# Kernel tuning notes

Hardware: AMD Instinct MI355X
Metric: run time of the kernel (lower is better)

The kernel has to match this reference:

```python
import jax, jax.numpy as jnp
import numpy as np

B, S, H, NH, K = 8, 1024, 1024, 16, 512
HD = H // NH  # head dim = 64


def setup_inputs() -> dict:
    key = jax.random.key(0)
    ks = jax.random.split(key, 9)
    hidden_states = jax.random.normal(ks[0], (B, S, H), jnp.float32)
    # remain_layers: exactly K nonzero entries per row (static max_tokens = K)
    scores = jax.random.uniform(ks[1], (B, S))
    thresh = jnp.sort(scores, axis=1)[:, S - K][:, None]
    remain_layers = (scores >= thresh).astype(jnp.int32)
    attention_mask = jnp.zeros((B, 1, 1, S), jnp.float32)  # additive mask
    init = 0.02
    Wq = jax.random.normal(ks[2], (H, H), jnp.float32) * init
    bq = jnp.zeros((H,), jnp.float32)
    Wk = jax.random.normal(ks[3], (H, H), jnp.float32) * init
    bk = jnp.zeros((H,), jnp.float32)
    Wv = jax.random.normal(ks[4], (H, H), jnp.float32) * init
    bv = jnp.zeros((H,), jnp.float32)
    return {"hidden_states": hidden_states, "attention_mask": attention_mask,
            "remain_layers": remain_layers, "Wq": Wq, "bq": bq,
            "Wk": Wk, "bk": bk, "Wv": Wv, "bv": bv}


def _heads(x):  # [B, L, H] -> [B, NH, L, HD]
    b, l, _ = x.shape
    return x.reshape(b, l, NH, HD).transpose(0, 2, 1, 3)


def reference(hidden_states, attention_mask, remain_layers, Wq, bq, Wk, bk, Wv, bv):
    # get_reduced_hidden: per-row gather of tokens with remain_layers > 0,
    # in original position order, zero-padded to max_tokens (= K here).
    order = jnp.argsort(1 - remain_layers, axis=1, stable=True)  # nonzeros first, order kept
    idx = order[:, :K]                                           # [B, K]
    reduced = jnp.take_along_axis(hidden_states, idx[:, :, None], axis=1)  # [B, K, H]
    valid = (jnp.take_along_axis(remain_layers, idx, axis=1) > 0)
    reduced = reduced * valid[:, :, None].astype(reduced.dtype)  # zero-pad slots

    q = _heads(reduced @ Wq.T + bq)          # [B, NH, K, HD]
    k = _heads(hidden_states @ Wk.T + bk)    # [B, NH, S, HD]
    v = _heads(hidden_states @ Wv.T + bv)    # [B, NH, S, HD]

    scores = jnp.einsum('bhqd,bhkd->bhqk', q, k) / np.sqrt(HD).astype(np.float32)
    scores = scores + attention_mask         # additive mask broadcast
    probs = jax.nn.softmax(scores, axis=-1)  # dropout is identity at eval
    ctx = jnp.einsum('bhqk,bhkd->bhqd', probs, v)  # [B, NH, K, HD]
    ctx = ctx.transpose(0, 2, 1, 3).reshape(B, K, H)
    return ctx
```

## Files before the change

### kernel.cpp

```cpp
#include <hip/hip_runtime.h>
#include <hip/hip_bf16.h>
#include <stdint.h>

#define S_LEN 1024
#define HDIM  1024
#define NHEADS 16
#define HEAD_D 64
#define KSEL  512
#define BATCH 8

typedef unsigned short ushort_t;
typedef __attribute__((ext_vector_type(8))) __bf16 bf16x8;
typedef __attribute__((ext_vector_type(4))) float  f32x4;

typedef const __attribute__((address_space(1))) void cg_void;
typedef __attribute__((address_space(3))) void lds_void;

__device__ __forceinline__ void gl_lds16(const void* g, void* l) {
    __builtin_amdgcn_global_load_lds((cg_void*)g, (lds_void*)l, 16, 0, 0);
}

__device__ __forceinline__ ushort_t f2bf(float f) {
    union { float f; unsigned int i; } x; x.f = f;
    unsigned int r = (x.i + 0x7fffu + ((x.i >> 16) & 1u)) >> 16;
    return (ushort_t)r;
}

__global__ __launch_bounds__(1024) void prep_kernel(
    const float* __restrict__ hidden, const float* __restrict__ wq,
    const float* __restrict__ wk, const float* __restrict__ wv,
    const int* __restrict__ remain,
    ushort_t* __restrict__ hbf, ushort_t* __restrict__ wqb,
    ushort_t* __restrict__ wkb, ushort_t* __restrict__ wvb,
    short* __restrict__ pos, int* __restrict__ valid) {
    __shared__ int wsum[16];
    __shared__ int woff[17];
    int blk = blockIdx.x;
    if (blk < 2816) {
        const float* s; ushort_t* d; int base;
        if (blk < 2048)      { s = hidden; d = hbf; base = blk; }
        else if (blk < 2304) { s = wq; d = wqb; base = blk - 2048; }
        else if (blk < 2560) { s = wk; d = wkb; base = blk - 2304; }
        else                 { s = wv; d = wvb; base = blk - 2560; }
        int i = base * 1024 + threadIdx.x;
        float4 v = ((const float4*)s)[i];
        ushort4 o;
        o.x = f2bf(v.x); o.y = f2bf(v.y); o.z = f2bf(v.z); o.w = f2bf(v.w);
        ((ushort4*)d)[i] = o;
    } else {
        int b = blk - 2816, t = threadIdx.x;
        int r = remain[b * S_LEN + t];
        unsigned long long m = __ballot(r != 0);
        int lane = t & 63, w = t >> 6;
        int pre = __popcll(m & ((1ull << lane) - 1ull));
        if (lane == 0) wsum[w] = __popcll(m);
        __syncthreads();
        if (t == 0) { int a = 0; for (int i = 0; i < 16; i++) { woff[i] = a; a += wsum[i]; } woff[16] = a; }
        __syncthreads();
        int tot = woff[16];
        int onesBefore = woff[w] + pre;
        int slot = r ? onesBefore : (tot + (t - onesBefore));
        pos[b * S_LEN + t] = (short)((slot < KSEL) ? slot : -1);
        if (slot < KSEL) valid[b * KSEL + slot] = r;
    }
}

#define QSCALE 0.1803368801111244f
#define LT_PITCH 264
#define BAR() __asm__ volatile("s_barrier" ::: "memory")
#define VMCNT(n) __asm__ volatile("s_waitcnt vmcnt(" #n ")" ::: "memory")

#define GPHASE(mt0, ...) { \
    bf16x8 Af0, Af1, Af2, Af3; \
    { const ushort_t* ap = &pool[Ab + (mt0) * 1024 + aRow]; \
      Af0 = *(const bf16x8*)(ap + ksw0); \
      Af1 = *(const bf16x8*)(ap + ksw1); \
      Af2 = *(const bf16x8*)(ap + 1024 + ksw0); \
      Af3 = *(const bf16x8*)(ap + 1024 + ksw1); } \
    __VA_ARGS__; \
    BAR(); \
    __builtin_amdgcn_s_setprio(1); \
    _Pragma("unroll") for (int nt = 0; nt < 4; nt++) \
        acc[mt0][nt]   = __builtin_amdgcn_mfma_f32_16x16x32_bf16(Af0, Bf[nt][0], acc[mt0][nt], 0, 0, 0); \
    _Pragma("unroll") for (int nt = 0; nt < 4; nt++) \
        acc[mt0+1][nt] = __builtin_amdgcn_mfma_f32_16x16x32_bf16(Af2, Bf[nt][0], acc[mt0+1][nt], 0, 0, 0); \
    _Pragma("unroll") for (int nt = 0; nt < 4; nt++) \
        acc[mt0][nt]   = __builtin_amdgcn_mfma_f32_16x16x32_bf16(Af1, Bf[nt][1], acc[mt0][nt], 0, 0, 0); \
    _Pragma("unroll") for (int nt = 0; nt < 4; nt++) \
        acc[mt0+1][nt] = __builtin_amdgcn_mfma_f32_16x16x32_bf16(Af3, Bf[nt][1], acc[mt0+1][nt], 0, 0, 0); \
    __builtin_amdgcn_s_setprio(0); \
    __builtin_amdgcn_sched_barrier(0); \
    BAR(); }

__global__ __launch_bounds__(512, 2) void gemm8(
    const ushort_t* __restrict__ hbf, const ushort_t* __restrict__ wkvq,
    const float* __restrict__ bk, const float* __restrict__ bv,
    const float* __restrict__ bq,
    const short* __restrict__ pos, const int* __restrict__ valid,
    ushort_t* __restrict__ kp, ushort_t* __restrict__ vt, ushort_t* __restrict__ qp) {
    __shared__ __align__(16) ushort_t pool[65536];
    const int i = blockIdx.x;
    const int swz = (i & 7) * 48 + (i >> 3);
    const int bmI = swz / 12, bnI = swz % 12;
    const int bm = bmI * 256;
    const int bn = bnI * 256;

    const int tid = threadIdx.x;
    const int lane = tid & 63;
    const int w = tid >> 6;
    const int quad = lane >> 4;
    const int cl = lane & 15;
    const int wr = w >> 2;
    const int wc = w & 3;

    const int r0 = tid >> 3;
    const int csw = ((tid & 7) ^ (r0 & 7)) * 8;
    const ushort_t* aSrc = hbf  + (bm + r0) * 1024 + csw;
    const ushort_t* bSrc = wkvq + (bn + r0) * 1024 + csw;

    const int aRow = cl * 64;
    const int ksw0 = (quad ^ (cl & 7)) * 8;
    const int ksw1 = ksw0 ^ 32;
    const int BbW = 32768 + (wc & 1) * 4096;
    const int BhT = wc >> 1;

    auto stageA = [&](int kt, int half) {
        const ushort_t* s = aSrc + half * 131072 + kt * 64;
        ushort_t* d = &pool[((kt & 1) * 2 + half) * 8192 + tid * 8];
        gl_lds16(s, d);
        gl_lds16(s + 65536, d + 4096);
    };
    auto stageB = [&](int kt, int half) {
        const ushort_t* s = bSrc + half * 131072 + kt * 64;
        ushort_t* d = &pool[32768 + ((kt & 1) * 2 + half) * 8192 + tid * 8];
        gl_lds16(s, d);
        gl_lds16(s + 65536, d + 4096);
    };

    f32x4 acc[8][4] = {};

    stageA(0, 0); stageA(0, 1);
    stageB(0, 0); stageB(0, 1);
    stageB(1, 0); stageB(1, 1);
    VMCNT(4);
    BAR();

    for (int u = 0; u < 16; ++u) {
        const int buf = u & 1;
        const int Ab = (buf * 2 + wr) * 8192;
        const int Bb = BbW + (buf * 2 + BhT) * 8192;

        bf16x8 Bf[4][2];
#pragma unroll
        for (int nt = 0; nt < 4; nt++) {
            const ushort_t* bp = &pool[Bb + nt * 1024 + aRow];
            Bf[nt][0] = *(const bf16x8*)(bp + ksw0);
            Bf[nt][1] = *(const bf16x8*)(bp + ksw1);
        }
        GPHASE(0, { if (u < 15) { stageA(u + 1, 0); stageA(u + 1, 1); } })
        GPHASE(2, { if (u < 14) stageB(u + 2, 0); })
        GPHASE(4, { if (u < 14) stageB(u + 2, 1); })
        GPHASE(6, { if (u < 14) { VMCNT(4); } else { VMCNT(0); } })
    }

    const int row0 = bm + wr * 128;
    const int colW = wc * 64;
    if (bnI < 4) {
        const int cb = bn + colW;
#pragma unroll
        for (int nt = 0; nt < 4; nt++) {
            int col = cb + nt * 16 + cl;
            float bb = bk[col];
#pragma unroll
            for (int mt = 0; mt < 8; mt++) {
                int rw = row0 + mt * 16 + quad * 4;
#pragma unroll
                for (int r = 0; r < 4; r++)
                    kp[(rw + r) * 1024 + col] = f2bf(acc[mt][nt][r] + bb);
            }
        }
    } else if (bnI < 8) {
        const int vcb = bn - 1024;
        const int b_ = bm >> 10;
        const int s0 = bm & 1023;
#pragma unroll
        for (int p2 = 0; p2 < 2; p2++) {
            if ((wc >> 1) == p2) {
#pragma unroll
                for (int nt = 0; nt < 4; nt++) {
                    int cloc = (wc & 1) * 64 + nt * 16 + cl;
                    float bb = bv[vcb + p2 * 128 + cloc];
#pragma unroll
                    for (int mt = 0; mt < 8; mt++) {
                        int rr = wr * 128 + mt * 16 + quad * 4;
#pragma unroll
                        for (int r = 0; r < 4; r++)
                            pool[cloc * LT_PITCH + rr + r] = f2bf(acc[mt][nt][r] + bb);
                    }
                }
            }
            __syncthreads();
            {
                int col = tid >> 2;
                int sq = tid & 3;
                int gb = ((b_ << 10) + vcb + p2 * 128 + col) * 1024 + s0;
                const ushort_t* src = &pool[col * LT_PITCH];
#pragma unroll
                for (int j = 0; j < 8; j++) {
                    int ch = (sq + 4 * j) * 8;
                    *(bf16x8*)(vt + gb + ch) = *(const bf16x8*)(src + ch);
                }
            }
            __syncthreads();
        }
    } else {
        const int qcb = bn - 2048 + colW;
        float bqv[4];
#pragma unroll
        for (int nt = 0; nt < 4; nt++) bqv[nt] = bq[qcb + nt * 16 + cl];
#pragma unroll
        for (int mt = 0; mt < 8; mt++) {
#pragma unroll
            for (int r = 0; r < 4; r++) {
                int row = row0 + mt * 16 + quad * 4 + r;
                int p = pos[row];
                if (p >= 0) {
                    float vm = (float)valid[((row >> 10) << 9) + p];
                    int ob = ((row >> 10) * 512 + p) * 1024 + qcb;
#pragma unroll
                    for (int nt = 0; nt < 4; nt++)
                        qp[ob + nt * 16 + cl] = f2bf((acc[mt][nt][r] * vm + bqv[nt]) * QSCALE);
                }
            }
        }
    }
}

#define P_PITCH 72
__global__ __launch_bounds__(256, 2) void attn_kernel(
    const ushort_t* __restrict__ qp, const ushort_t* __restrict__ kp,
    const ushort_t* __restrict__ vt, const float* __restrict__ mask,
    float* __restrict__ out) {
    __shared__ __align__(16) ushort_t ks[2][4096];
    __shared__ __align__(16) ushort_t vs[2][4096];
    __shared__ __align__(16) ushort_t ps[4][32 * P_PITCH];
    const int tid = threadIdx.x;
    const int lane = tid & 63;
    const int w = tid >> 6;
    const int quad = lane >> 4;
    const int cl = lane & 15;
    const int qt = blockIdx.x, h = blockIdx.y, b = blockIdx.z;

    const int srow = tid >> 2;
    const int fsa = ((tid >> 2) & 3) ^ ((tid >> 4) & 3);
    const int sc8 = ((tid & 3) ^ fsa) * 8;
    const int lds_off = tid * 8;
    const int fr = (cl & 3) ^ ((cl >> 2) & 3);
    const int qo = (quad ^ fr) * 8;

    const long kbase = (long)b * S_LEN;
    const long vbase = (long)b * 1024 + h * HEAD_D;

    const long qrow0 = (long)b * KSEL + qt * 128 + w * 32;
    bf16x8 aq[2][2];
#pragma unroll
    for (int mt = 0; mt < 2; mt++)
#pragma unroll
        for (int kk = 0; kk < 2; kk++)
            aq[mt][kk] = *(const bf16x8*)(qp + (qrow0 + mt * 16 + cl) * HDIM + h * HEAD_D + kk * 32 + quad * 8);

    f32x4 O[2][4] = {};
    float l_r[2][4] = {};

#pragma unroll
    for (int j = 0; j < 2; j++) {
        gl_lds16(kp + (kbase + srow) * (long)HDIM + h * HEAD_D + j * 32 + sc8, &ks[0][j * 2048 + lds_off]);
        gl_lds16(vt + (vbase + srow) * (long)S_LEN + j * 32 + sc8, &vs[0][j * 2048 + lds_off]);
    }

    for (int c = 0; c < S_LEN / 64; c++) {
        __asm__ volatile("s_waitcnt vmcnt(0)" ::: "memory");
        __syncthreads();
        if (c + 1 < S_LEN / 64) {
            int nb = (c + 1) & 1;
#pragma unroll
            for (int j = 0; j < 2; j++) {
                gl_lds16(kp + (kbase + (c + 1) * 64 + srow) * (long)HDIM + h * HEAD_D + j * 32 + sc8,
                         &ks[nb][j * 2048 + lds_off]);
                gl_lds16(vt + (vbase + srow) * (long)S_LEN + (c + 1) * 64 + j * 32 + sc8,
                         &vs[nb][j * 2048 + lds_off]);
            }
        }
        const ushort_t* kbuf = ks[c & 1];
        const ushort_t* vbuf = vs[c & 1];

        f32x4 sc[2][4] = {};
#pragma unroll
        for (int kk = 0; kk < 2; kk++)
#pragma unroll
            for (int nt = 0; nt < 4; nt++) {
                bf16x8 bk8 = *(const bf16x8*)&kbuf[kk * 2048 + (nt * 16 + cl) * 32 + qo];
#pragma unroll
                for (int mt = 0; mt < 2; mt++)
                    sc[mt][nt] = __builtin_amdgcn_mfma_f32_16x16x32_bf16(aq[mt][kk], bk8, sc[mt][nt], 0, 0, 0);
            }

#pragma unroll
        for (int nt = 0; nt < 4; nt++) {
            float mv = mask[b * S_LEN + c * 64 + nt * 16 + cl] * 1.44269504f;
#pragma unroll
            for (int mt = 0; mt < 2; mt++)
#pragma unroll
                for (int r = 0; r < 4; r++) {
                    float p_ = __builtin_amdgcn_exp2f(sc[mt][nt][r] + mv);
                    sc[mt][nt][r] = p_;
                    l_r[mt][r] += p_;
                }
        }

#pragma unroll
        for (int mt = 0; mt < 2; mt++)
#pragma unroll
            for (int nt = 0; nt < 4; nt++)
#pragma unroll
                for (int r = 0; r < 4; r++)
                    ps[w][(mt * 16 + quad * 4 + r) * P_PITCH + nt * 16 + cl] = f2bf(sc[mt][nt][r]);

        __asm__ volatile("s_waitcnt lgkmcnt(0)" ::: "memory");

#pragma unroll
        for (int kk = 0; kk < 2; kk++) {
            bf16x8 ap[2];
#pragma unroll
            for (int mt = 0; mt < 2; mt++)
                ap[mt] = *(const bf16x8*)&ps[w][(mt * 16 + cl) * P_PITCH + kk * 32 + quad * 8];
#pragma unroll
            for (int dt = 0; dt < 4; dt++) {
                bf16x8 bv8 = *(const bf16x8*)&vbuf[kk * 2048 + (dt * 16 + cl) * 32 + qo];
#pragma unroll
                for (int mt = 0; mt < 2; mt++)
                    O[mt][dt] = __builtin_amdgcn_mfma_f32_16x16x32_bf16(ap[mt], bv8, O[mt][dt], 0, 0, 0);
            }
        }
    }

#pragma unroll
    for (int mt = 0; mt < 2; mt++)
#pragma unroll
        for (int r = 0; r < 4; r++) {
            float s0 = l_r[mt][r];
#pragma unroll
            for (int d = 1; d < 16; d <<= 1) s0 += __shfl_xor(s0, d, 64);
            l_r[mt][r] = s0;
        }

#pragma unroll
    for (int mt = 0; mt < 2; mt++) {
        const long orow0 = qrow0 + mt * 16 + quad * 4;
#pragma unroll
        for (int dt = 0; dt < 4; dt++) {
            int col = h * HEAD_D + dt * 16 + cl;
#pragma unroll
            for (int r = 0; r < 4; r++)
                out[(orow0 + r) * HDIM + col] = O[mt][dt][r] / l_r[mt][r];
        }
    }
}

extern "C" void kernel_launch(void* const* d_in, const int* in_sizes, int n_in,
                              void* d_out, int out_size, void* d_ws, size_t ws_size,
                              hipStream_t stream) {
    const float* hidden = (const float*)d_in[0];
    const float* mask   = (const float*)d_in[1];
    const int*   remain = (const int*)d_in[2];
    const float* Wq = (const float*)d_in[3];
    const float* bq = (const float*)d_in[4];
    const float* Wk = (const float*)d_in[5];
    const float* bk = (const float*)d_in[6];
    const float* Wv = (const float*)d_in[7];
    const float* bv = (const float*)d_in[8];
    float* out = (float*)d_out;

    char* ws = (char*)d_ws;
    size_t off = 0;
    short* pos   = (short*)(ws + off); off += 16384;
    int* valid = (int*)(ws + off); off += 16384;
    ushort_t* hbf  = (ushort_t*)(ws + off); off += (size_t)BATCH * S_LEN * HDIM * 2;
    ushort_t* wkvq = (ushort_t*)(ws + off); off += (size_t)3 * HDIM * HDIM * 2;
    ushort_t* qp  = (ushort_t*)(ws + off); off += (size_t)BATCH * KSEL * HDIM * 2;
    ushort_t* kp  = (ushort_t*)(ws + off); off += (size_t)BATCH * S_LEN * HDIM * 2;
    ushort_t* vt  = (ushort_t*)(ws + off); off += (size_t)BATCH * S_LEN * HDIM * 2;

    prep_kernel<<<2824, 1024, 0, stream>>>(hidden, Wq, Wk, Wv, remain,
                                           hbf, wkvq + 2 * 1048576, wkvq,
                                           wkvq + 1048576, pos, valid);
    gemm8<<<384, 512, 0, stream>>>(hbf, wkvq, bk, bv, bq, pos, valid, kp, vt, qp);
    attn_kernel<<<dim3(4, NHEADS, BATCH), 256, 0, stream>>>(qp, kp, vt, mask, out);
}
```

Measured before the change: 203.9 us.

## Restructure QKV GEMM mainloop to 4-stage K=32 pipeline; stage mask in LDS

The QKV projection GEMM drops its hand-scheduled two-buffer K=64 loop, which had split phases, priority hints and several barriers per step. In its place is a four-slot ring of K=32 tiles prefetched three steps ahead, with one barrier per step and a simpler XOR swizzle. This is meant to hide global-to-LDS load latency with deeper prefetch and fewer barriers, at the cost of more loop iterations and losing the explicit MFMA/load interleaving. The attention kernel also preloads the additive mask, pre-scaled by log2(e), into shared memory once per block so the inner loop reads LDS instead of global memory.

Result: slower. 211.2 us (+3.6%).

```diff
diff --git a/kernel.cpp b/kernel.cpp
--- a/kernel.cpp
+++ b/kernel.cpp
@@ -70,28 +70,6 @@
 #define BAR() __asm__ volatile("s_barrier" ::: "memory")
 #define VMCNT(n) __asm__ volatile("s_waitcnt vmcnt(" #n ")" ::: "memory")
 
-#define GPHASE(mt0, ...) { \
-    bf16x8 Af0, Af1, Af2, Af3; \
-    { const ushort_t* ap = &pool[Ab + (mt0) * 1024 + aRow]; \
-      Af0 = *(const bf16x8*)(ap + ksw0); \
-      Af1 = *(const bf16x8*)(ap + ksw1); \
-      Af2 = *(const bf16x8*)(ap + 1024 + ksw0); \
-      Af3 = *(const bf16x8*)(ap + 1024 + ksw1); } \
-    __VA_ARGS__; \
-    BAR(); \
-    __builtin_amdgcn_s_setprio(1); \
-    _Pragma("unroll") for (int nt = 0; nt < 4; nt++) \
-        acc[mt0][nt]   = __builtin_amdgcn_mfma_f32_16x16x32_bf16(Af0, Bf[nt][0], acc[mt0][nt], 0, 0, 0); \
-    _Pragma("unroll") for (int nt = 0; nt < 4; nt++) \
-        acc[mt0+1][nt] = __builtin_amdgcn_mfma_f32_16x16x32_bf16(Af2, Bf[nt][0], acc[mt0+1][nt], 0, 0, 0); \
-    _Pragma("unroll") for (int nt = 0; nt < 4; nt++) \
-        acc[mt0][nt]   = __builtin_amdgcn_mfma_f32_16x16x32_bf16(Af1, Bf[nt][1], acc[mt0][nt], 0, 0, 0); \
-    _Pragma("unroll") for (int nt = 0; nt < 4; nt++) \
-        acc[mt0+1][nt] = __builtin_amdgcn_mfma_f32_16x16x32_bf16(Af3, Bf[nt][1], acc[mt0+1][nt], 0, 0, 0); \
-    __builtin_amdgcn_s_setprio(0); \
-    __builtin_amdgcn_sched_barrier(0); \
-    BAR(); }
-
 __global__ __launch_bounds__(512, 2) void gemm8(
     const ushort_t* __restrict__ hbf, const ushort_t* __restrict__ wkvq,
     const float* __restrict__ bk, const float* __restrict__ bv,
@@ -113,54 +91,49 @@
     const int wr = w >> 2;
     const int wc = w & 3;
 
-    const int r0 = tid >> 3;
-    const int csw = ((tid & 7) ^ (r0 & 7)) * 8;
-    const ushort_t* aSrc = hbf  + (bm + r0) * 1024 + csw;
-    const ushort_t* bSrc = wkvq + (bn + r0) * 1024 + csw;
-
-    const int aRow = cl * 64;
-    const int ksw0 = (quad ^ (cl & 7)) * 8;
-    const int ksw1 = ksw0 ^ 32;
-    const int BbW = 32768 + (wc & 1) * 4096;
-    const int BhT = wc >> 1;
-
-    auto stageA = [&](int kt, int half) {
-        const ushort_t* s = aSrc + half * 131072 + kt * 64;
-        ushort_t* d = &pool[((kt & 1) * 2 + half) * 8192 + tid * 8];
-        gl_lds16(s, d);
-        gl_lds16(s + 65536, d + 4096);
+    const int sr = tid >> 2;
+    const int scol = ((tid & 3) ^ (sr & 3)) * 8;
+    const ushort_t* aSrc = hbf  + (bm + sr) * 1024 + scol;
+    const ushort_t* bSrc = wkvq + (bn + sr) * 1024 + scol;
+    const int dOff = tid * 8;
+
+    const int ksw = (quad ^ (cl & 3)) * 8;
+    const int aR0 = wr * 128;
+    const int bR0 = wc * 64;
+
+    auto stage = [&](int kt) {
+        const int sl = (kt & 3) * 8192;
+        const ushort_t* sa = aSrc + kt * 32;
+        const ushort_t* sb = bSrc + kt * 32;
+        gl_lds16(sa,                &pool[sl + dOff]);
+        gl_lds16(sa + 131072,       &pool[sl + 4096 + dOff]);
+        gl_lds16(sb,                &pool[32768 + sl + dOff]);
+        gl_lds16(sb + 131072,       &pool[32768 + sl + 4096 + dOff]);
     };
-    auto stageB = [&](int kt, int half) {
-        const ushort_t* s = bSrc + half * 131072 + kt * 64;
-        ushort_t* d = &pool[32768 + ((kt & 1) * 2 + half) * 8192 + tid * 8];
-        gl_lds16(s, d);
-        gl_lds16(s + 65536, d + 4096);
-    };
 
     f32x4 acc[8][4] = {};
 
-    stageA(0, 0); stageA(0, 1);
-    stageB(0, 0); stageB(0, 1);
-    stageB(1, 0); stageB(1, 1);
-    VMCNT(4);
-    BAR();
-
-    for (int u = 0; u < 16; ++u) {
-        const int buf = u & 1;
-        const int Ab = (buf * 2 + wr) * 8192;
-        const int Bb = BbW + (buf * 2 + BhT) * 8192;
-
-        bf16x8 Bf[4][2];
-#pragma unroll
-        for (int nt = 0; nt < 4; nt++) {
-            const ushort_t* bp = &pool[Bb + nt * 1024 + aRow];
-            Bf[nt][0] = *(const bf16x8*)(bp + ksw0);
-            Bf[nt][1] = *(const bf16x8*)(bp + ksw1);
-        }
-        GPHASE(0, { if (u < 15) { stageA(u + 1, 0); stageA(u + 1, 1); } })
-        GPHASE(2, { if (u < 14) stageB(u + 2, 0); })
-        GPHASE(4, { if (u < 14) stageB(u + 2, 1); })
-        GPHASE(6, { if (u < 14) { VMCNT(4); } else { VMCNT(0); } })
+    stage(0); stage(1); stage(2);
+    VMCNT(8);
+
+    for (int u = 0; u < 32; ++u) {
+        BAR();
+        if (u < 29) stage(u + 3);
+        const int sl = (u & 3) * 8192;
+        bf16x8 bf[4];
+#pragma unroll
+        for (int nt = 0; nt < 4; nt++)
+            bf[nt] = *(const bf16x8*)&pool[32768 + sl + (bR0 + nt * 16 + cl) * 32 + ksw];
+#pragma unroll
+        for (int mt = 0; mt < 8; mt++) {
+            bf16x8 af = *(const bf16x8*)&pool[sl + (aR0 + mt * 16 + cl) * 32 + ksw];
+#pragma unroll
+            for (int nt = 0; nt < 4; nt++)
+                acc[mt][nt] = __builtin_amdgcn_mfma_f32_16x16x32_bf16(af, bf[nt], acc[mt][nt], 0, 0, 0);
+        }
+        if (u < 29)      VMCNT(8);
+        else if (u == 29) VMCNT(4);
+        else if (u == 30) VMCNT(0);
     }
 
     const int row0 = bm + wr * 128;
@@ -244,6 +217,7 @@
     __shared__ __align__(16) ushort_t ks[2][4096];
     __shared__ __align__(16) ushort_t vs[2][4096];
     __shared__ __align__(16) ushort_t ps[4][32 * P_PITCH];
+    __shared__ float mlds[1024];
     const int tid = threadIdx.x;
     const int lane = tid & 63;
     const int w = tid >> 6;
@@ -261,6 +235,14 @@
     const long kbase = (long)b * S_LEN;
     const long vbase = (long)b * 1024 + h * HEAD_D;
 
+    {
+        float4 mv4 = *(const float4*)(mask + b * S_LEN + tid * 4);
+        mlds[tid * 4 + 0] = mv4.x * 1.44269504f;
+        mlds[tid * 4 + 1] = mv4.y * 1.44269504f;
+        mlds[tid * 4 + 2] = mv4.z * 1.44269504f;
+        mlds[tid * 4 + 3] = mv4.w * 1.44269504f;
+    }
+
     const long qrow0 = (long)b * KSEL + qt * 128 + w * 32;
     bf16x8 aq[2][2];
 #pragma unroll
@@ -307,7 +289,7 @@
 
 #pragma unroll
         for (int nt = 0; nt < 4; nt++) {
-            float mv = mask[b * S_LEN + c * 64 + nt * 16 + cl] * 1.44269504f;
+            float mv = mlds[c * 64 + nt * 16 + cl];
 #pragma unroll
             for (int mt = 0; mt < 2; mt++)
 #pragma unroll
```
